# Kernel optimization log

Hardware: AMD Instinct MI355X
Metric: run time of the kernel (lower is better)

Reference implementation:

```python
import jax, jax.numpy as jnp
import numpy as np


def setup_inputs() -> dict:
    key = jax.random.key(0)
    x = jax.random.normal(key, (4096, 4096), dtype=jnp.float32)
    return {"x": x}


def reference(x):
    """IDXST: y_k = Im{ sum_{n=0}^{N-1} x_n * exp(j*pi*n*(2k+1)/(2N)) }.

    O(N log N) via a 2N-point FFT:
      sum_n x_n e^{j pi n (2k+1)/(2N)} = sum_n (x_n e^{j pi n/(2N)}) e^{j 2 pi n k/(2N)}
    which is the first N entries of an unnormalized 2N-point inverse DFT of the
    twiddled, zero-padded sequence.
    """
    N = x.shape[-1]
    n = jnp.arange(N)
    twiddle = jnp.exp(1j * jnp.pi * n.astype(jnp.float32) / (2.0 * N)).astype(jnp.complex64)
    c = x.astype(jnp.complex64) * twiddle                      # [..., N]
    pad = [(0, 0)] * (x.ndim - 1) + [(0, N)]
    c = jnp.pad(c, pad)                                        # [..., 2N]
    y = jnp.fft.ifft(c, axis=-1) * (2.0 * N)                   # unnormalized IDFT
    return jnp.imag(y[..., :N]).astype(x.dtype)
```

## Files before the change

kernel.cpp:

```cpp
#include <hip/hip_runtime.h>
#include <stdint.h>


#define NN 4096

typedef __attribute__((ext_vector_type(8))) short short8;
typedef __attribute__((ext_vector_type(4))) float f32x4;

__device__ __forceinline__ unsigned short f2bf(float f) {
  unsigned int u = __float_as_uint(f);
  u += 0x7fffu + ((u >> 16) & 1u);
  return (unsigned short)(u >> 16);
}

__device__ __forceinline__ void async_load16(const void* g, void* lds) {
  __builtin_amdgcn_global_load_lds(
      (const __attribute__((address_space(1))) unsigned int*)g,
      (__attribute__((address_space(3))) unsigned int*)lds, 16, 0, 0);
}

#define NXS (NN * NN / 8)
#define NBO (2048 * 2048 / 4)
#define NBP (1024 * 1024 / 4)

__global__ void prep_kernel(const float* __restrict__ x,
                            unsigned short* __restrict__ xo,
                            unsigned short* __restrict__ xee,
                            unsigned short* __restrict__ xeo,
                            unsigned short* __restrict__ Bo,
                            unsigned short* __restrict__ Bp,
                            unsigned short* __restrict__ Bq) {
  int gi = blockIdx.x * blockDim.x + threadIdx.x;
  if (gi < NXS) {
    int g = gi & 511;
    int r = gi >> 9;
    const float4* src = (const float4*)(x + (size_t)r * NN + g * 8);
    float4 v0 = src[0], v1 = src[1];
    ushort4 ov;
    ov.x = f2bf(v0.y); ov.y = f2bf(v0.w); ov.z = f2bf(v1.y); ov.w = f2bf(v1.w);
    *(ushort4*)&xo[(size_t)r * 2048 + g * 4] = ov;
    unsigned int ee = ((unsigned)f2bf(v1.x) << 16) | f2bf(v0.x);
    *(unsigned int*)&xee[(size_t)r * 1024 + g * 2] = ee;
    unsigned int eo = ((unsigned)f2bf(v1.z) << 16) | f2bf(v0.z);
    *(unsigned int*)&xeo[(size_t)r * 1024 + g * 2] = eo;
  } else if (gi < NXS + NBO) {
    int i = gi - NXS;
    int m0 = (i & 511) * 4;
    int c = i >> 9;
    unsigned int tw = 2u * (unsigned)c + 1u;
    const float sc = 3.14159265358979323846f / 8192.0f;
    ushort4 o; unsigned int ph;
    ph = ((unsigned)(2 * (m0 + 0) + 1) * tw) & 16383u; o.x = f2bf(__sinf((float)ph * sc));
    ph = ((unsigned)(2 * (m0 + 1) + 1) * tw) & 16383u; o.y = f2bf(__sinf((float)ph * sc));
    ph = ((unsigned)(2 * (m0 + 2) + 1) * tw) & 16383u; o.z = f2bf(__sinf((float)ph * sc));
    ph = ((unsigned)(2 * (m0 + 3) + 1) * tw) & 16383u; o.w = f2bf(__sinf((float)ph * sc));
    *(ushort4*)&Bo[(size_t)c * 2048 + m0] = o;
  } else if (gi < NXS + NBO + NBP) {
    int i = gi - NXS - NBO;
    int t0 = (i & 255) * 4;
    int c = i >> 8;
    unsigned int tw = 2u * (unsigned)c + 1u;
    const float sc = 3.14159265358979323846f / 2048.0f;
    ushort4 o; unsigned int ph;
    ph = ((unsigned)(t0 + 0) * tw) & 4095u; o.x = f2bf(__sinf((float)ph * sc));
    ph = ((unsigned)(t0 + 1) * tw) & 4095u; o.y = f2bf(__sinf((float)ph * sc));
    ph = ((unsigned)(t0 + 2) * tw) & 4095u; o.z = f2bf(__sinf((float)ph * sc));
    ph = ((unsigned)(t0 + 3) * tw) & 4095u; o.w = f2bf(__sinf((float)ph * sc));
    *(ushort4*)&Bp[(size_t)c * 1024 + t0] = o;
  } else {
    int i = gi - NXS - NBO - NBP;
    int t0 = (i & 255) * 4;
    int c = i >> 8;
    unsigned int tw = 2u * (unsigned)c + 1u;
    const float sc = 3.14159265358979323846f / 4096.0f;
    ushort4 o; unsigned int ph;
    ph = ((unsigned)(2 * (t0 + 0) + 1) * tw) & 8191u; o.x = f2bf(__sinf((float)ph * sc));
    ph = ((unsigned)(2 * (t0 + 1) + 1) * tw) & 8191u; o.y = f2bf(__sinf((float)ph * sc));
    ph = ((unsigned)(2 * (t0 + 2) + 1) * tw) & 8191u; o.z = f2bf(__sinf((float)ph * sc));
    ph = ((unsigned)(2 * (t0 + 3) + 1) * tw) & 8191u; o.w = f2bf(__sinf((float)ph * sc));
    *(ushort4*)&Bq[(size_t)c * 1024 + t0] = o;
  }
}

#define PH_BAR  __builtin_amdgcn_s_barrier()
#define W_LGKM0 asm volatile("s_waitcnt lgkmcnt(0)" ::: "memory")
#define W_VM5   asm volatile("s_waitcnt vmcnt(5)" ::: "memory")
#define W_VM0   asm volatile("s_waitcnt vmcnt(0)" ::: "memory")
#define PRIO1   __builtin_amdgcn_s_setprio(1)
#define PRIO0   __builtin_amdgcn_s_setprio(0)

#define STAGEA_G(Abase, Kc, prow0, koff, off) do {                              \
    const unsigned short* _s =                                                  \
        (Abase) + (size_t)((prow0) + st_r) * (Kc) + (koff) + st_c;              \
    async_load16(_s, &lds[(off) + tid * 8]);                                    \
    async_load16(_s + (size_t)64 * (Kc), &lds[(off) + 4096 + tid * 8]);         \
  } while (0)

#define STAGEB_P(srcp, koff, off)                                               \
    async_load16((srcp) + (koff), &lds[(off) + tid * 8])

#define LOADA_G(base, b, mh) do {                                               \
    const int _ab = (base) + (b) * 16384 + wm * 4096 + (mh) * 2048 + lr * 64;   \
    _Pragma("unroll") for (int _i = 0; _i < 2; ++_i) {                          \
      av[(mh) * 2 + _i][0] = *(const short8*)&lds[_ab + _i * 1024 + cA0];       \
      av[(mh) * 2 + _i][1] = *(const short8*)&lds[_ab + _i * 1024 + cA1];       \
    }                                                                           \
  } while (0)

#define LOADB_U(SET, nh) do {                                                   \
    const int _bb = 65536 + wn * 4096 + (nh) * 2048 + lr * 64;                  \
    _Pragma("unroll") for (int _j = 0; _j < 2; ++_j) {                          \
      SET[_j][0] = *(const short8*)&lds[_bb + _j * 1024 + cA0];                 \
      SET[_j][1] = *(const short8*)&lds[_bb + _j * 1024 + cA1];                 \
    }                                                                           \
  } while (0)

#define LOADB_PQ(SET, base) do {                                                \
    const int _bb = (base) + wn * 2048 + lr * 64;                               \
    _Pragma("unroll") for (int _j = 0; _j < 2; ++_j) {                          \
      SET[_j][0] = *(const short8*)&lds[_bb + _j * 1024 + cA0];                 \
      SET[_j][1] = *(const short8*)&lds[_bb + _j * 1024 + cA1];                 \
    }                                                                           \
  } while (0)

#define MMAQ_U(BS, mh, nh) do {                                                 \
    _Pragma("unroll") for (int _k = 0; _k < 2; ++_k)                            \
    _Pragma("unroll") for (int _i = 0; _i < 2; ++_i)                            \
    _Pragma("unroll") for (int _j = 0; _j < 2; ++_j)                            \
      uacc[(mh) * 2 + _i][(nh) * 2 + _j] =                                      \
          __builtin_amdgcn_mfma_f32_16x16x32_bf16(                              \
              av[(mh) * 2 + _i][_k], BS[_j][_k],                                \
              uacc[(mh) * 2 + _i][(nh) * 2 + _j], 0, 0, 0);                     \
  } while (0)

#define MMAQ_PQ(ACC, BS, mh) do {                                               \
    _Pragma("unroll") for (int _k = 0; _k < 2; ++_k)                            \
    _Pragma("unroll") for (int _i = 0; _i < 2; ++_i)                            \
    _Pragma("unroll") for (int _j = 0; _j < 2; ++_j)                            \
      ACC[(mh) * 2 + _i][_j] =                                                  \
          __builtin_amdgcn_mfma_f32_16x16x32_bf16(                              \
              av[(mh) * 2 + _i][_k], BS[_j][_k],                                \
              ACC[(mh) * 2 + _i][_j], 0, 0, 0);                                 \
  } while (0)

__global__ __launch_bounds__(512) void gemm3_kernel(
    const unsigned short* __restrict__ xo,
    const unsigned short* __restrict__ xee,
    const unsigned short* __restrict__ xeo,
    const unsigned short* __restrict__ Bo,
    const unsigned short* __restrict__ Bp,
    const unsigned short* __restrict__ Bq,
    float* __restrict__ out) {
  __shared__ __align__(16) unsigned short lds[73728];

  const int bx = blockIdx.x;
  const int row0 = (bx & 15) * 256;
  const int c0 = (bx >> 4) * 32;

  const int tid = threadIdx.x;
  const int lane = tid & 63;
  const int wave = tid >> 6;
  const int wm = wave >> 1;
  const int wn = wave & 1;
  const int lr = lane & 15, kq = lane >> 4;
  const int st_r = tid >> 3;
  const int st_c = ((tid & 7) ^ (st_r & 7)) * 8;
  const int cA0 = (kq ^ (lr & 7)) * 8;
  const int cA1 = ((4 + kq) ^ (lr & 7)) * 8;

  const int ru0 = (st_r < 32) ? (c0 + st_r) : (2047 - c0 - (st_r - 32));
  const int ru1 = (st_r < 32) ? (1023 - c0 - st_r) : (1024 + c0 + (st_r - 32));
  const int rpq = (st_r < 32) ? (c0 + st_r) : (1023 - c0 - (st_r - 32));
  const unsigned short* sBo0 = Bo + (size_t)ru0 * 2048 + st_c;
  const unsigned short* sBo1 = Bo + (size_t)ru1 * 2048 + st_c;
  const unsigned short* sBp  = Bp + (size_t)rpq * 1024 + st_c;
  const unsigned short* sBq  = Bq + (size_t)rpq * 1024 + st_c;

  f32x4 uacc[4][4], pacc[4][2], qacc[4][2];
#pragma unroll
  for (int i = 0; i < 4; ++i) {
#pragma unroll
    for (int j = 0; j < 4; ++j) uacc[i][j] = (f32x4){0.f, 0.f, 0.f, 0.f};
#pragma unroll
    for (int j = 0; j < 2; ++j) {
      pacc[i][j] = (f32x4){0.f, 0.f, 0.f, 0.f};
      qacc[i][j] = (f32x4){0.f, 0.f, 0.f, 0.f};
    }
  }
  short8 av[4][2], bv0[2][2], bv1[2][2];

  STAGEA_G(xo, 2048, row0,       0, 0);
  STAGEA_G(xo, 2048, row0 + 128, 0, 8192);
  STAGEB_P(sBo0, 0, 65536);
  STAGEB_P(sBo1, 0, 69632);
  W_VM0; PH_BAR;

  for (int it = 0; it < 15; ++it) {
    const int t64 = it << 7;
    LOADA_G(0, 0, 0); LOADB_U(bv0, 0);
    STAGEA_G(xo, 2048, row0, t64 + 64, 16384);
    W_LGKM0; PRIO1; MMAQ_U(bv0, 0, 0); PRIO0; PH_BAR;
    LOADB_U(bv1, 1);
    STAGEA_G(xo, 2048, row0 + 128, t64 + 64, 24576);
    W_LGKM0; PRIO1; MMAQ_U(bv1, 0, 1); PRIO0; PH_BAR;
    LOADA_G(0, 0, 1);
    STAGEB_P(sBo0, t64 + 64, 65536);
    STAGEB_P(sBo1, t64 + 64, 69632);
    W_LGKM0; PRIO1; MMAQ_U(bv1, 1, 1); PRIO0; PH_BAR;
    PRIO1; MMAQ_U(bv0, 1, 0); PRIO0; W_VM0; PH_BAR;
    LOADA_G(0, 1, 0); LOADB_U(bv0, 0);
    STAGEA_G(xo, 2048, row0, t64 + 128, 0);
    W_LGKM0; PRIO1; MMAQ_U(bv0, 0, 0); PRIO0; PH_BAR;
    LOADB_U(bv1, 1);
    STAGEA_G(xo, 2048, row0 + 128, t64 + 128, 8192);
    W_LGKM0; PRIO1; MMAQ_U(bv1, 0, 1); PRIO0; PH_BAR;
    LOADA_G(0, 1, 1);
    STAGEB_P(sBo0, t64 + 128, 65536);
    STAGEB_P(sBo1, t64 + 128, 69632);
    W_LGKM0; PRIO1; MMAQ_U(bv1, 1, 1); PRIO0; PH_BAR;
    PRIO1; MMAQ_U(bv0, 1, 0); PRIO0; W_VM0; PH_BAR;
  }
  {
    LOADA_G(0, 0, 0); LOADB_U(bv0, 0);
    STAGEA_G(xo, 2048, row0, 1984, 16384);
    W_LGKM0; PRIO1; MMAQ_U(bv0, 0, 0); PRIO0; PH_BAR;
    LOADB_U(bv1, 1);
    STAGEA_G(xo, 2048, row0 + 128, 1984, 24576);
    W_LGKM0; PRIO1; MMAQ_U(bv1, 0, 1); PRIO0; PH_BAR;
    LOADA_G(0, 0, 1);
    STAGEB_P(sBo0, 1984, 65536);
    STAGEB_P(sBo1, 1984, 69632);
    W_LGKM0; PRIO1; MMAQ_U(bv1, 1, 1); PRIO0; PH_BAR;
    PRIO1; MMAQ_U(bv0, 1, 0); PRIO0; W_VM0; PH_BAR;
    LOADA_G(0, 1, 0); LOADB_U(bv0, 0);
    W_LGKM0; PRIO1; MMAQ_U(bv0, 0, 0); PRIO0;
    LOADB_U(bv1, 1);
    W_LGKM0; PRIO1; MMAQ_U(bv1, 0, 1); PRIO0;
    LOADA_G(0, 1, 1);
    W_LGKM0; PRIO1; MMAQ_U(bv1, 1, 1); MMAQ_U(bv0, 1, 0); PRIO0;
  }

  PH_BAR;
  STAGEA_G(xee, 1024, row0,       0, 0);
  STAGEA_G(xee, 1024, row0 + 128, 0, 8192);
  STAGEB_P(sBp, 0, 65536);
  STAGEA_G(xeo, 1024, row0,       0, 32768);
  STAGEA_G(xeo, 1024, row0 + 128, 0, 40960);
  STAGEB_P(sBq, 0, 69632);
  W_VM5; PH_BAR;

#define PQ_TILE(b, kn) do {                                                     \
    LOADA_G(0, b, 0); LOADB_PQ(bv0, 65536);                                     \
    STAGEA_G(xee, 1024, row0, kn, ((b) ^ 1) * 16384);                           \
    W_LGKM0; PRIO1; MMAQ_PQ(pacc, bv0, 0); PRIO0; PH_BAR;                       \
    LOADA_G(0, b, 1);                                                           \
    STAGEA_G(xee, 1024, row0 + 128, kn, ((b) ^ 1) * 16384 + 8192);              \
    STAGEB_P(sBp, kn, 65536);                                                   \
    W_LGKM0; PRIO1; MMAQ_PQ(pacc, bv0, 1); PRIO0; W_VM5; PH_BAR;                \
    LOADA_G(32768, b, 0); LOADB_PQ(bv1, 69632);                                 \
    STAGEA_G(xeo, 1024, row0, kn, 32768 + ((b) ^ 1) * 16384);                   \
    W_LGKM0; PRIO1; MMAQ_PQ(qacc, bv1, 0); PRIO0; PH_BAR;                       \
    LOADA_G(32768, b, 1);                                                       \
    STAGEA_G(xeo, 1024, row0 + 128, kn, 32768 + ((b) ^ 1) * 16384 + 8192);      \
    STAGEB_P(sBq, kn, 69632);                                                   \
    W_LGKM0; PRIO1; MMAQ_PQ(qacc, bv1, 1); PRIO0; W_VM5; PH_BAR;                \
  } while (0)

  for (int it = 0; it < 7; ++it) {
    const int t64 = it << 7;
    PQ_TILE(0, t64 + 64);
    PQ_TILE(1, t64 + 128);
  }
  PQ_TILE(0, 960);
  {
    LOADA_G(0, 1, 0); LOADB_PQ(bv0, 65536);
    W_LGKM0; PRIO1; MMAQ_PQ(pacc, bv0, 0); PRIO0;
    LOADA_G(0, 1, 1);
    W_LGKM0; PRIO1; MMAQ_PQ(pacc, bv0, 1); PRIO0; W_VM0; PH_BAR;
    LOADA_G(32768, 1, 0); LOADB_PQ(bv1, 69632);
    W_LGKM0; PRIO1; MMAQ_PQ(qacc, bv1, 0); PRIO0;
    LOADA_G(32768, 1, 1);
    W_LGKM0; PRIO1; MMAQ_PQ(qacc, bv1, 1); PRIO0;
  }
#undef PQ_TILE

#pragma unroll
  for (int i = 0; i < 4; ++i)
#pragma unroll
    for (int j = 0; j < 2; ++j)
#pragma unroll
      for (int rr = 0; rr < 4; ++rr) {
        const int r_out = row0 + wm * 64 + i * 16 + kq * 4 + rr;
        float* orow = out + (size_t)r_out * NN;
        const int cs = j * 16 + lr;
        const float u1 = uacc[i][j][rr];
        const float u4 = uacc[i][j + 2][rr];
        const float pa = pacc[i][j][rr];
        const float qa = qacc[i][j][rr];
        const float v1 = pa + qa;
        const float v2 = qa - pa;
        if (wn == 0) {
          orow[c0 + cs]        = v1 + u1;
          orow[4095 - c0 - cs] = u1 - v1;
          orow[2047 - c0 - cs] = v2 + u4;
          orow[2048 + c0 + cs] = u4 - v2;
        } else {
          orow[1023 - c0 - cs] = v1 + u1;
          orow[3072 + c0 + cs] = u1 - v1;
          orow[1024 + c0 + cs] = v2 + u4;
          orow[3071 - c0 - cs] = u4 - v2;
        }
      }
}

extern "C" void kernel_launch(void* const* d_in, const int* in_sizes, int n_in,
                              void* d_out, int out_size, void* d_ws, size_t ws_size,
                              hipStream_t stream) {
  const float* x = (const float*)d_in[0];
  float* out = (float*)d_out;
  unsigned short* xo  = (unsigned short*)d_ws;
  unsigned short* xee = xo + (size_t)NN * 2048;
  unsigned short* xeo = xee + (size_t)NN * 1024;
  unsigned short* Bo  = xeo + (size_t)NN * 1024;
  unsigned short* Bp  = Bo + (size_t)2048 * 2048;
  unsigned short* Bq  = Bp + (size_t)1024 * 1024;

  int prep_threads = NXS + NBO + 2 * NBP;
  prep_kernel<<<prep_threads / 256, 256, 0, stream>>>(x, xo, xee, xeo, Bo, Bp, Bq);

  gemm3_kernel<<<256, 512, 0, stream>>>(xo, xee, xeo, Bo, Bp, Bq, out);
}
```

Baseline: 78.28 us.

## Restructure GEMM main loop into triple-buffered LDS pipeline with fewer barriers

Replaces the double-buffered, finely interleaved load/MFMA schedule with a three-stage LDS ring (A and B buffers), so each tile's global loads are issued two stages ahead. It uses one barrier per K-step instead of several, and drops the explicit lgkmcnt waits, relying on the compiler instead. The P and Q passes become sequential streams through the same ring rather than being interleaved. This aims to hide global latency and cut synchronisation overhead. The cost is a larger prefetch depth, more registers (an extra B fragment set), and relying on correct vmcnt counts for safety.

```diff
diff --git a/kernel.cpp b/kernel.cpp
--- a/kernel.cpp
+++ b/kernel.cpp
@@ -82,8 +82,15 @@
   }
 }
 
+#define AB0 0
+#define AB1 16384
+#define AB2 32768
+#define BB0 49152
+#define BB1 57344
+#define BB2 65536
+
 #define PH_BAR  __builtin_amdgcn_s_barrier()
-#define W_LGKM0 asm volatile("s_waitcnt lgkmcnt(0)" ::: "memory")
+#define W_VM6   asm volatile("s_waitcnt vmcnt(6)" ::: "memory")
 #define W_VM5   asm volatile("s_waitcnt vmcnt(5)" ::: "memory")
 #define W_VM0   asm volatile("s_waitcnt vmcnt(0)" ::: "memory")
 #define PRIO1   __builtin_amdgcn_s_setprio(1)
@@ -99,24 +106,24 @@
 #define STAGEB_P(srcp, koff, off)                                               \
     async_load16((srcp) + (koff), &lds[(off) + tid * 8])
 
-#define LOADA_G(base, b, mh) do {                                               \
-    const int _ab = (base) + (b) * 16384 + wm * 4096 + (mh) * 2048 + lr * 64;   \
+#define LOADA3(ab, mh) do {                                                     \
+    const int _ab = (ab) + wm * 4096 + (mh) * 2048 + lr * 64;                   \
     _Pragma("unroll") for (int _i = 0; _i < 2; ++_i) {                          \
       av[(mh) * 2 + _i][0] = *(const short8*)&lds[_ab + _i * 1024 + cA0];       \
       av[(mh) * 2 + _i][1] = *(const short8*)&lds[_ab + _i * 1024 + cA1];       \
     }                                                                           \
   } while (0)
 
-#define LOADB_U(SET, nh) do {                                                   \
-    const int _bb = 65536 + wn * 4096 + (nh) * 2048 + lr * 64;                  \
+#define LOADBU3(SET, bb, nh) do {                                               \
+    const int _bb = (bb) + wn * 4096 + (nh) * 2048 + lr * 64;                   \
     _Pragma("unroll") for (int _j = 0; _j < 2; ++_j) {                          \
       SET[_j][0] = *(const short8*)&lds[_bb + _j * 1024 + cA0];                 \
       SET[_j][1] = *(const short8*)&lds[_bb + _j * 1024 + cA1];                 \
     }                                                                           \
   } while (0)
 
-#define LOADB_PQ(SET, base) do {                                                \
-    const int _bb = (base) + wn * 2048 + lr * 64;                               \
+#define LOADBP3(SET, bb) do {                                                   \
+    const int _bb = (bb) + wn * 2048 + lr * 64;                                 \
     _Pragma("unroll") for (int _j = 0; _j < 2; ++_j) {                          \
       SET[_j][0] = *(const short8*)&lds[_bb + _j * 1024 + cA0];                 \
       SET[_j][1] = *(const short8*)&lds[_bb + _j * 1024 + cA1];                 \
@@ -142,6 +149,36 @@
               av[(mh) * 2 + _i][_k], BS[_j][_k],                                \
               ACC[(mh) * 2 + _i][_j], 0, 0, 0);                                 \
   } while (0)
+
+#define U_CORE(ab, bb)                                                          \
+    LOADA3(ab, 0); LOADA3(ab, 1);                                               \
+    LOADBU3(bv0, bb, 0); LOADBU3(bv1, bb, 1)
+
+#define U_MMA                                                                   \
+    PRIO1; MMAQ_U(bv0, 0, 0); MMAQ_U(bv1, 0, 1);                                \
+    MMAQ_U(bv1, 1, 1); MMAQ_U(bv0, 1, 0); PRIO0
+
+#define STG_U(an, bn, kn)                                                       \
+    STAGEA_G(xo, 2048, row0, kn, an);                                           \
+    STAGEA_G(xo, 2048, row0 + 128, kn, (an) + 8192);                            \
+    STAGEB_P(sBo0, kn, bn);                                                     \
+    STAGEB_P(sBo1, kn, (bn) + 4096)
+
+#define STG_P(an, bn, kn)                                                       \
+    STAGEA_G(xee, 1024, row0, kn, an);                                          \
+    STAGEA_G(xee, 1024, row0 + 128, kn, (an) + 8192);                           \
+    STAGEB_P(sBp, kn, bn)
+
+#define STG_Q(an, bn, kn)                                                       \
+    STAGEA_G(xeo, 1024, row0, kn, an);                                          \
+    STAGEA_G(xeo, 1024, row0 + 128, kn, (an) + 8192);                           \
+    STAGEB_P(sBq, kn, bn)
+
+#define PQ_CORE(ab, bb)                                                         \
+    LOADA3(ab, 0); LOADA3(ab, 1); LOADBP3(bvp, bb)
+
+#define PQ_MMA(ACC)                                                             \
+    PRIO1; MMAQ_PQ(ACC, bvp, 0); MMAQ_PQ(ACC, bvp, 1); PRIO0
 
 __global__ __launch_bounds__(512) void gemm3_kernel(
     const unsigned short* __restrict__ xo,
@@ -187,102 +224,42 @@
       qacc[i][j] = (f32x4){0.f, 0.f, 0.f, 0.f};
     }
   }
-  short8 av[4][2], bv0[2][2], bv1[2][2];
-
-  STAGEA_G(xo, 2048, row0,       0, 0);
-  STAGEA_G(xo, 2048, row0 + 128, 0, 8192);
-  STAGEB_P(sBo0, 0, 65536);
-  STAGEB_P(sBo1, 0, 69632);
-  W_VM0; PH_BAR;
-
-  for (int it = 0; it < 15; ++it) {
-    const int t64 = it << 7;
-    LOADA_G(0, 0, 0); LOADB_U(bv0, 0);
-    STAGEA_G(xo, 2048, row0, t64 + 64, 16384);
-    W_LGKM0; PRIO1; MMAQ_U(bv0, 0, 0); PRIO0; PH_BAR;
-    LOADB_U(bv1, 1);
-    STAGEA_G(xo, 2048, row0 + 128, t64 + 64, 24576);
-    W_LGKM0; PRIO1; MMAQ_U(bv1, 0, 1); PRIO0; PH_BAR;
-    LOADA_G(0, 0, 1);
-    STAGEB_P(sBo0, t64 + 64, 65536);
-    STAGEB_P(sBo1, t64 + 64, 69632);
-    W_LGKM0; PRIO1; MMAQ_U(bv1, 1, 1); PRIO0; PH_BAR;
-    PRIO1; MMAQ_U(bv0, 1, 0); PRIO0; W_VM0; PH_BAR;
-    LOADA_G(0, 1, 0); LOADB_U(bv0, 0);
-    STAGEA_G(xo, 2048, row0, t64 + 128, 0);
-    W_LGKM0; PRIO1; MMAQ_U(bv0, 0, 0); PRIO0; PH_BAR;
-    LOADB_U(bv1, 1);
-    STAGEA_G(xo, 2048, row0 + 128, t64 + 128, 8192);
-    W_LGKM0; PRIO1; MMAQ_U(bv1, 0, 1); PRIO0; PH_BAR;
-    LOADA_G(0, 1, 1);
-    STAGEB_P(sBo0, t64 + 128, 65536);
-    STAGEB_P(sBo1, t64 + 128, 69632);
-    W_LGKM0; PRIO1; MMAQ_U(bv1, 1, 1); PRIO0; PH_BAR;
-    PRIO1; MMAQ_U(bv0, 1, 0); PRIO0; W_VM0; PH_BAR;
-  }
-  {
-    LOADA_G(0, 0, 0); LOADB_U(bv0, 0);
-    STAGEA_G(xo, 2048, row0, 1984, 16384);
-    W_LGKM0; PRIO1; MMAQ_U(bv0, 0, 0); PRIO0; PH_BAR;
-    LOADB_U(bv1, 1);
-    STAGEA_G(xo, 2048, row0 + 128, 1984, 24576);
-    W_LGKM0; PRIO1; MMAQ_U(bv1, 0, 1); PRIO0; PH_BAR;
-    LOADA_G(0, 0, 1);
-    STAGEB_P(sBo0, 1984, 65536);
-    STAGEB_P(sBo1, 1984, 69632);
-    W_LGKM0; PRIO1; MMAQ_U(bv1, 1, 1); PRIO0; PH_BAR;
-    PRIO1; MMAQ_U(bv0, 1, 0); PRIO0; W_VM0; PH_BAR;
-    LOADA_G(0, 1, 0); LOADB_U(bv0, 0);
-    W_LGKM0; PRIO1; MMAQ_U(bv0, 0, 0); PRIO0;
-    LOADB_U(bv1, 1);
-    W_LGKM0; PRIO1; MMAQ_U(bv1, 0, 1); PRIO0;
-    LOADA_G(0, 1, 1);
-    W_LGKM0; PRIO1; MMAQ_U(bv1, 1, 1); MMAQ_U(bv0, 1, 0); PRIO0;
-  }
-
-  PH_BAR;
-  STAGEA_G(xee, 1024, row0,       0, 0);
-  STAGEA_G(xee, 1024, row0 + 128, 0, 8192);
-  STAGEB_P(sBp, 0, 65536);
-  STAGEA_G(xeo, 1024, row0,       0, 32768);
-  STAGEA_G(xeo, 1024, row0 + 128, 0, 40960);
-  STAGEB_P(sBq, 0, 69632);
-  W_VM5; PH_BAR;
-
-#define PQ_TILE(b, kn) do {                                                     \
-    LOADA_G(0, b, 0); LOADB_PQ(bv0, 65536);                                     \
-    STAGEA_G(xee, 1024, row0, kn, ((b) ^ 1) * 16384);                           \
-    W_LGKM0; PRIO1; MMAQ_PQ(pacc, bv0, 0); PRIO0; PH_BAR;                       \
-    LOADA_G(0, b, 1);                                                           \
-    STAGEA_G(xee, 1024, row0 + 128, kn, ((b) ^ 1) * 16384 + 8192);              \
-    STAGEB_P(sBp, kn, 65536);                                                   \
-    W_LGKM0; PRIO1; MMAQ_PQ(pacc, bv0, 1); PRIO0; W_VM5; PH_BAR;                \
-    LOADA_G(32768, b, 0); LOADB_PQ(bv1, 69632);                                 \
-    STAGEA_G(xeo, 1024, row0, kn, 32768 + ((b) ^ 1) * 16384);                   \
-    W_LGKM0; PRIO1; MMAQ_PQ(qacc, bv1, 0); PRIO0; PH_BAR;                       \
-    LOADA_G(32768, b, 1);                                                       \
-    STAGEA_G(xeo, 1024, row0 + 128, kn, 32768 + ((b) ^ 1) * 16384 + 8192);      \
-    STAGEB_P(sBq, kn, 69632);                                                   \
-    W_LGKM0; PRIO1; MMAQ_PQ(qacc, bv1, 1); PRIO0; W_VM5; PH_BAR;                \
-  } while (0)
-
-  for (int it = 0; it < 7; ++it) {
-    const int t64 = it << 7;
-    PQ_TILE(0, t64 + 64);
-    PQ_TILE(1, t64 + 128);
-  }
-  PQ_TILE(0, 960);
-  {
-    LOADA_G(0, 1, 0); LOADB_PQ(bv0, 65536);
-    W_LGKM0; PRIO1; MMAQ_PQ(pacc, bv0, 0); PRIO0;
-    LOADA_G(0, 1, 1);
-    W_LGKM0; PRIO1; MMAQ_PQ(pacc, bv0, 1); PRIO0; W_VM0; PH_BAR;
-    LOADA_G(32768, 1, 0); LOADB_PQ(bv1, 69632);
-    W_LGKM0; PRIO1; MMAQ_PQ(qacc, bv1, 0); PRIO0;
-    LOADA_G(32768, 1, 1);
-    W_LGKM0; PRIO1; MMAQ_PQ(qacc, bv1, 1); PRIO0;
-  }
-#undef PQ_TILE
+  short8 av[4][2], bv0[2][2], bv1[2][2], bvp[2][2];
+
+  STG_U(AB0, BB0, 0);
+  STG_U(AB1, BB1, 64);
+  W_VM6; PH_BAR;
+
+  for (int it = 0; it < 10; ++it) {
+    const int kb = it * 192;
+    U_CORE(AB0, BB0); STG_U(AB2, BB2, kb + 128); U_MMA; W_VM6; PH_BAR;
+    U_CORE(AB1, BB1); STG_U(AB0, BB0, kb + 192); U_MMA; W_VM6; PH_BAR;
+    U_CORE(AB2, BB2); STG_U(AB1, BB1, kb + 256); U_MMA; W_VM6; PH_BAR;
+  }
+  U_CORE(AB0, BB0); STG_P(AB2, BB2, 0); U_MMA; W_VM5; PH_BAR;
+  U_CORE(AB1, BB1); STG_P(AB0, BB0, 64); U_MMA; W_VM5; PH_BAR;
+
+  for (int it = 0; it < 4; ++it) {
+    const int kb = it * 192;
+    PQ_CORE(AB2, BB2); STG_P(AB1, BB1, kb + 128); PQ_MMA(pacc); W_VM5; PH_BAR;
+    PQ_CORE(AB0, BB0); STG_P(AB2, BB2, kb + 192); PQ_MMA(pacc); W_VM5; PH_BAR;
+    PQ_CORE(AB1, BB1); STG_P(AB0, BB0, kb + 256); PQ_MMA(pacc); W_VM5; PH_BAR;
+  }
+  PQ_CORE(AB2, BB2); STG_P(AB1, BB1, 896); PQ_MMA(pacc); W_VM5; PH_BAR;
+  PQ_CORE(AB0, BB0); STG_P(AB2, BB2, 960); PQ_MMA(pacc); W_VM5; PH_BAR;
+  PQ_CORE(AB1, BB1); STG_Q(AB0, BB0, 0);   PQ_MMA(pacc); W_VM5; PH_BAR;
+  PQ_CORE(AB2, BB2); STG_Q(AB1, BB1, 64);  PQ_MMA(pacc); W_VM5; PH_BAR;
+
+  for (int it = 0; it < 4; ++it) {
+    const int kb = it * 192;
+    PQ_CORE(AB0, BB0); STG_Q(AB2, BB2, kb + 128); PQ_MMA(qacc); W_VM5; PH_BAR;
+    PQ_CORE(AB1, BB1); STG_Q(AB0, BB0, kb + 192); PQ_MMA(qacc); W_VM5; PH_BAR;
+    PQ_CORE(AB2, BB2); STG_Q(AB1, BB1, kb + 256); PQ_MMA(qacc); W_VM5; PH_BAR;
+  }
+  PQ_CORE(AB0, BB0); STG_Q(AB2, BB2, 896); PQ_MMA(qacc); W_VM5; PH_BAR;
+  PQ_CORE(AB1, BB1); STG_Q(AB0, BB0, 960); PQ_MMA(qacc); W_VM5; PH_BAR;
+  PQ_CORE(AB2, BB2); PQ_MMA(qacc); W_VM0; PH_BAR;
+  PQ_CORE(AB0, BB0); PQ_MMA(qacc);
 
 #pragma unroll
   for (int i = 0; i < 4; ++i)
```

New measurement: 76.53 us. -2.2%, faster.
